# Kernel tuning notes

Hardware: AMD Instinct MI355X
Metric: run time of the kernel (lower is better)

Reference implementation:

```python
import jax, jax.numpy as jnp
import numpy as np
from jax import lax

D_MAX = 6.4; GRID_RES = 0.1; G = 9.81; MASS = 40.0
K_STIFF = 5000.0; K_DAMP = float(np.sqrt(4.0 * MASS * K_STIFF)); K_FRIC = 0.5
DT = 0.01; N_STEPS = 500; EPS = 1e-6


def _robot_geometry():
    # DPhysConfig.rigid_body_geometry(from_mesh=False), robot_size=(1.0, 0.5)
    xs = np.concatenate([np.linspace(-0.5, 0.5, 8), np.linspace(-0.5, 0.5, 8)])
    ys = np.concatenate([0.25 * np.ones(8), -0.25 * np.ones(8)])
    zz = np.array([0.2, 0.1, 0.0, 0.0, 0.0, 0.0, 0.1, 0.2])
    zs = np.concatenate([zz, zz])
    pts = np.stack([xs, ys, zs], 1).astype(np.float32)
    cog = pts.mean(0)
    return pts, (pts[:, 1] > cog[1]), (pts[:, 1] < cog[1])


def _inertia_inv(mass, pts):
    n = pts.shape[0]; mp = mass / n
    x, y, z = pts[:, 0], pts[:, 1], pts[:, 2]
    Ixx = (mp * (y**2 + z**2)).sum(); Iyy = (mp * (x**2 + z**2)).sum(); Izz = (mp * (x**2 + y**2)).sum()
    Ixy = -(mp * x * y).sum(); Ixz = -(mp * x * z).sum(); Iyz = -(mp * y * z).sum()
    I = np.array([[Ixx, Ixy, Ixz], [Ixy, Iyy, Iyz], [Ixz, Iyz, Izz]], dtype=np.float64) * 10.0
    return np.linalg.inv(I).astype(np.float32)


def _interp(grid, xq, yq):
    # bilinear interpolation of (B,H,W) grid at metric query points (B,N)
    B, H, W = grid.shape
    xi = jnp.clip((xq + D_MAX) / GRID_RES, 0.0, H - 2)
    yi = jnp.clip((yq + D_MAX) / GRID_RES, 0.0, W - 2)
    x0 = jnp.floor(xi).astype(jnp.int32); y0 = jnp.floor(yi).astype(jnp.int32)
    b = jnp.arange(B)[:, None]
    z00 = grid[b, x0, y0];     z10 = grid[b, x0 + 1, y0]
    z01 = grid[b, x0, y0 + 1]; z11 = grid[b, x0 + 1, y0 + 1]
    wx = xi - x0; wy = yi - y0
    return z00 * (1 - wx) * (1 - wy) + z10 * wx * (1 - wy) + z01 * (1 - wx) * wy + z11 * wx * wy


def _normals(grid, xq, yq):
    e = GRID_RES
    dzdx = (_interp(grid, xq + e, yq) - _interp(grid, xq - e, yq)) / (2 * e)
    dzdy = (_interp(grid, xq, yq + e) - _interp(grid, xq, yq - e)) / (2 * e)
    n = jnp.stack([-dzdx, -dzdy, jnp.ones_like(dzdx)], -1)
    return n / (jnp.linalg.norm(n, axis=-1, keepdims=True) + EPS)


def _skew(v):
    z = jnp.zeros_like(v[..., 0])
    return jnp.stack([
        jnp.stack([z, -v[..., 2], v[..., 1]], -1),
        jnp.stack([v[..., 2], z, -v[..., 0]], -1),
        jnp.stack([-v[..., 1], v[..., 0], z], -1)], -2)


def _rk4(x, xd, dt):
    k1 = dt * xd
    k2 = dt * (xd + k1 / 2)
    k3 = dt * (xd + k2 / 2)
    k4 = dt * (xd + k3)
    return x + (k1 + 2 * k2 + 2 * k3 + k4) / 6


def _integrate_rotation(R, omega, dt):
    Ox = _skew(omega)                                  # (B,3,3)
    theta = jnp.linalg.norm(omega, axis=-1)[:, None, None]
    Oxn = Ox / (theta + EPS)
    I3 = jnp.eye(3, dtype=R.dtype)
    return R @ (I3 + Oxn * jnp.sin(theta * dt) + (Oxn @ Oxn) * (1 - jnp.cos(theta * dt)))


def _forward_sim(z_grid, controls, robot_points, I_inv, mask_left, mask_right):
    B = z_grid.shape[0]; n_pts = robot_points.shape[0]
    dt = jnp.float32(DT)
    x = jnp.zeros((B, 3), z_grid.dtype).at[:, 2].set(1.0)
    xd = jnp.zeros((B, 3), z_grid.dtype)
    R = jnp.broadcast_to(jnp.eye(3, dtype=z_grid.dtype), (B, 3, 3))
    omega = jnp.zeros((B, 3), z_grid.dtype)
    x_points = x[:, None, :] + robot_points[None]      # (B,n,3)
    xd_points = jnp.zeros((B, n_pts, 3), z_grid.dtype)
    ml = mask_left[None, :, None]; mr = mask_right[None, :, None]

    def step(carry, u):
        x, xd, R, omega, x_points, xd_points = carry
        u_left, u_right = u[:, 0], u[:, 1]
        # --- forward_kinematics ---
        z_pts = _interp(z_grid, x_points[..., 0], x_points[..., 1])[..., None]
        dh = x_points[..., 2:3] - z_pts
        on_grid = ((x_points[..., 0:1] >= -D_MAX) & (x_points[..., 0:1] <= D_MAX) &
                   (x_points[..., 1:2] >= -D_MAX) & (x_points[..., 1:2] <= D_MAX))
        in_contact = ((dh <= 0.0) & on_grid).astype(x_points.dtype)
        n = _normals(z_grid, x_points[..., 0], x_points[..., 1])   # (B,n,3)
        xd_n = (xd_points * n).sum(-1, keepdims=True)
        F_spring = -(K_STIFF * dh + K_DAMP * xd_n) * n * in_contact
        thrust = R[..., 0]                                         # R @ [1,0,0]
        thrust = thrust / (jnp.linalg.norm(thrust, axis=-1, keepdims=True) + EPS)
        N = jnp.linalg.norm(F_spring, axis=2)[..., None]           # (B,n,1)
        v_l = (u_left[:, None] * thrust)[:, None, :]
        v_r = (u_right[:, None] * thrust)[:, None, :]
        f_l = K_FRIC * N * jnp.tanh(v_l - xd_points)
        f_r = K_FRIC * N * jnp.tanh(v_r - xd_points)
        F_fric = jnp.where(ml, f_l, jnp.where(mr, f_r, jnp.zeros_like(f_l)))
        r = x_points - x[:, None, :]
        torque = jnp.cross(r, F_spring + F_fric).sum(1)            # (B,3)
        omega_d = torque @ I_inv.T
        F_cog = jnp.array([0.0, 0.0, -MASS * G], z_grid.dtype) + F_spring.mean(1) + F_fric.mean(1)
        xdd = F_cog / MASS
        xd_pts_new = xd[:, None, :] + jnp.cross(omega[:, None, :], r)
        # --- update_state ---
        xd_new = _rk4(xd, xdd, dt)
        x_new = _rk4(x, xd_new, dt)
        x_points_new = _rk4(x_points, xd_pts_new, dt)
        omega_new = _rk4(omega, omega_d, dt)
        R_new = _integrate_rotation(R, omega_new, dt)
        carry_new = (x_new, xd_new, R_new, omega_new, x_points_new, xd_pts_new)
        out = jnp.concatenate([x_new, xd_new, omega_new, R_new.reshape(B, 9),
                               x_points_new.reshape(B, -1),
                               F_spring.reshape(B, -1), F_fric.reshape(B, -1)], -1)
        return carry_new, out

    _, traj = lax.scan(step, (x, xd, R, omega, x_points, xd_points),
                       jnp.swapaxes(controls, 0, 1))
    return jnp.swapaxes(traj, 0, 1)   # (B, T, 3+3+3+9+48+48+48=162)


def setup_inputs() -> dict:
    key = jax.random.key(0)
    k1, k2 = jax.random.split(key)
    B, H, W, T = 256, 128, 128, N_STEPS
    pts, ml, mr = _robot_geometry()
    z_grid = 0.1 * jax.random.normal(k1, (B, H, W), dtype=jnp.float32)
    controls = jax.random.uniform(k2, (B, T, 2), dtype=jnp.float32, minval=-1.2, maxval=1.2)
    return {
        "z_grid": z_grid,
        "controls": controls,
        "robot_points": jnp.asarray(pts),
        "I_inv": jnp.asarray(_inertia_inv(MASS, pts)),
        "mask_left": jnp.asarray(ml),
        "mask_right": jnp.asarray(mr),
    }


def reference(z_grid, controls, robot_points, I_inv, mask_left, mask_right):
    return _forward_sim(z_grid, controls, robot_points, I_inv, mask_left, mask_right)
```

## Files before the change

### kernel.cpp

```cpp
#include <hip/hip_runtime.h>
#include <math.h>

#define WGRID 128
#define HGRID 128
#define TSTEPS 500

__device__ __forceinline__ float dpp_sum16(float v) {
    int x;
    x = __builtin_amdgcn_update_dpp(0, __float_as_int(v), 0xB1, 0xF, 0xF, true);
    v += __int_as_float(x);
    x = __builtin_amdgcn_update_dpp(0, __float_as_int(v), 0x4E, 0xF, 0xF, true);
    v += __int_as_float(x);
    x = __builtin_amdgcn_update_dpp(0, __float_as_int(v), 0x141, 0xF, 0xF, true);
    v += __int_as_float(x);
    x = __builtin_amdgcn_update_dpp(0, __float_as_int(v), 0x140, 0xF, 0xF, true);
    v += __int_as_float(x);
    return v;
}

struct Ax { int i0; float w; };
__device__ __forceinline__ Ax axq(float q) {
    float xi = (q + 6.4f) / 0.1f;
    xi = fminf(fmaxf(xi, 0.0f), 126.0f);
    float f = floorf(xi);
    Ax a; a.i0 = (int)f; a.w = xi - f; return a;
}

struct Iq { float z00, z01, z10, z11, wx, wy; };
__device__ __forceinline__ Iq issueQ(const float* __restrict__ zb, Ax ax, Ax ay) {
    const float* r0 = zb + (ax.i0 * WGRID + ay.i0);
    Iq q;
    q.z00 = r0[0];
    q.z01 = r0[1];
    q.z10 = r0[WGRID];
    q.z11 = r0[WGRID + 1];
    q.wx = ax.w; q.wy = ay.w;
    return q;
}
__device__ __forceinline__ float combineQ(Iq q) {
    float ox = 1.0f - q.wx, oy = 1.0f - q.wy;
    return q.z00 * ox * oy + q.z10 * q.wx * oy + q.z01 * ox * q.wy + q.z11 * q.wx * q.wy;
}

extern "C" __global__ __launch_bounds__(64, 1) void dphys_sim(
    const float* __restrict__ z_grid,
    const float* __restrict__ controls,
    const float* __restrict__ robot_points,
    const float* __restrict__ I_inv,
    float* __restrict__ out)
{
    const int b = blockIdx.x;
    const int lane = threadIdx.x;

    const float* __restrict__ zb = z_grid + (size_t)b * (HGRID * WGRID);

    const float i00 = I_inv[0], i01 = I_inv[1], i02 = I_inv[2];
    const float i10 = I_inv[3], i11 = I_inv[4], i12 = I_inv[5];
    const float i20 = I_inv[6], i21 = I_inv[7], i22 = I_inv[8];

    const int p = lane & 15;
    const float rpx = robot_points[3 * p + 0];
    const float rpy = robot_points[3 * p + 1];
    const float rpz = robot_points[3 * p + 2];

    const float cog_y = dpp_sum16(rpy) * (1.0f / 16.0f);
    const bool is_left = rpy > cog_y;

    const float K_STIFF = 5000.0f;
    const float K_DAMP  = 894.4271909999159f;
    const float K_FRIC  = 0.5f;
    const float EPSF    = 1e-6f;
    const float CRK     = 0.010050166708416667f;

    float X = 0.f, Y = 0.f, Z = 1.f;
    float VX = 0.f, VY = 0.f, VZ = 0.f;
    float R00 = 1.f, R01 = 0.f, R02 = 0.f;
    float R10 = 0.f, R11 = 1.f, R12 = 0.f;
    float R20 = 0.f, R21 = 0.f, R22 = 1.f;
    float OX = 0.f, OY = 0.f, OZ = 0.f;
    float px = rpx, py = rpy, pz = rpz + 1.0f;
    float pvx = 0.f, pvy = 0.f, pvz = 0.f;

    float* outb = out + (size_t)b * TSTEPS * 162;
    const float* cg = controls + (size_t)b * (TSTEPS * 2);

    float u_l = cg[0], u_r = cg[1];

    Ax ax0 = axq(px), axp = axq(px + 0.1f), axm = axq(px - 0.1f);
    Ax ay0 = axq(py), ayp = axq(py + 0.1f), aym = axq(py - 0.1f);
    Iq qc  = issueQ(zb, ax0, ay0);
    Iq qxp = issueQ(zb, axp, ay0);
    Iq qxm = issueQ(zb, axm, ay0);
    Iq qyp = issueQ(zb, ax0, ayp);
    Iq qym = issueQ(zb, ax0, aym);

    #pragma unroll 1
    for (int t = 0; t < TSTEPS; ++t) {
        const int tn = (t + 1 < TSTEPS) ? (t + 1) : t;
        const float u_l_nxt = cg[2 * tn + 0];
        const float u_r_nxt = cg[2 * tn + 1];

        const float rx = px - X, ry = py - Y, rz = pz - Z;
        const float pvnx = VX + (OY * rz - OZ * ry);
        const float pvny = VY + (OZ * rx - OX * rz);
        const float pvnz = VZ + (OX * ry - OY * rx);
        const float pxn = fmaf(pvnx, CRK, px);
        const float pyn = fmaf(pvny, CRK, py);
        const float pzn = fmaf(pvnz, CRK, pz);

        Ax nax0 = axq(pxn), naxp = axq(pxn + 0.1f), naxm = axq(pxn - 0.1f);
        Ax nay0 = axq(pyn), nayp = axq(pyn + 0.1f), naym = axq(pyn - 0.1f);
        Iq nqc  = issueQ(zb, nax0, nay0);
        Iq nqxp = issueQ(zb, naxp, nay0);
        Iq nqxm = issueQ(zb, naxm, nay0);
        Iq nqyp = issueQ(zb, nax0, nayp);
        Iq nqym = issueQ(zb, nax0, naym);

        const float z_pt = combineQ(qc);
        const float zpx  = combineQ(qxp);
        const float zmx  = combineQ(qxm);
        const float zpy  = combineQ(qyp);
        const float zmy  = combineQ(qym);

        const float dh = pz - z_pt;
        const bool on = (px >= -6.4f) && (px <= 6.4f) && (py >= -6.4f) && (py <= 6.4f);
        const float contact = ((dh <= 0.0f) && on) ? 1.0f : 0.0f;

        const float dzdx = (zpx - zmx) / 0.2f;
        const float dzdy = (zpy - zmy) / 0.2f;
        float nx = -dzdx, ny = -dzdy, nz = 1.0f;
        const float nn = sqrtf(nx * nx + ny * ny + nz * nz) + EPSF;
        nx /= nn; ny /= nn; nz /= nn;

        const float xd_n = pvx * nx + pvy * ny + pvz * nz;
        const float s_mag = -(K_STIFF * dh + K_DAMP * xd_n);
        const float fsx = s_mag * nx * contact;
        const float fsy = s_mag * ny * contact;
        const float fsz = s_mag * nz * contact;

        const float Nmag = sqrtf(fsx * fsx + fsy * fsy + fsz * fsz);

        float tx = R00, ty = R10, tz = R20;
        const float tnn = sqrtf(tx * tx + ty * ty + tz * tz) + EPSF;
        tx /= tnn; ty /= tnn; tz /= tnn;

        const float u_sel = is_left ? u_l : u_r;
        const float kn = K_FRIC * Nmag;
        const float ffx = kn * tanhf(u_sel * tx - pvx);
        const float ffy = kn * tanhf(u_sel * ty - pvy);
        const float ffz = kn * tanhf(u_sel * tz - pvz);

        const float Fx = fsx + ffx, Fy = fsy + ffy, Fz = fsz + ffz;
        const float tqx = ry * Fz - rz * Fy;
        const float tqy = rz * Fx - rx * Fz;
        const float tqz = rx * Fy - ry * Fx;

        const float Tqx = dpp_sum16(tqx);
        const float Tqy = dpp_sum16(tqy);
        const float Tqz = dpp_sum16(tqz);
        const float Ssx = dpp_sum16(fsx);
        const float Ssy = dpp_sum16(fsy);
        const float Ssz = dpp_sum16(fsz);
        const float Sfx = dpp_sum16(ffx);
        const float Sfy = dpp_sum16(ffy);
        const float Sfz = dpp_sum16(ffz);

        const float odx = i00 * Tqx + i01 * Tqy + i02 * Tqz;
        const float ody = i10 * Tqx + i11 * Tqy + i12 * Tqz;
        const float odz = i20 * Tqx + i21 * Tqy + i22 * Tqz;

        const float Fcx = Ssx * 0.0625f + Sfx * 0.0625f;
        const float Fcy = Ssy * 0.0625f + Sfy * 0.0625f;
        const float Fcz = -392.4f + Ssz * 0.0625f + Sfz * 0.0625f;
        const float axd = Fcx / 40.0f;
        const float ayd = Fcy / 40.0f;
        const float azd = Fcz / 40.0f;

        const float VXn = fmaf(axd, CRK, VX);
        const float VYn = fmaf(ayd, CRK, VY);
        const float VZn = fmaf(azd, CRK, VZ);
        const float Xn = fmaf(VXn, CRK, X);
        const float Yn = fmaf(VYn, CRK, Y);
        const float Zn = fmaf(VZn, CRK, Z);
        const float OXn = fmaf(odx, CRK, OX);
        const float OYn = fmaf(ody, CRK, OY);
        const float OZn = fmaf(odz, CRK, OZ);

        const float th = sqrtf(OXn * OXn + OYn * OYn + OZn * OZn);
        const float tpe = th + EPSF;
        const float axn = OXn / tpe, ayn = OYn / tpe, azn = OZn / tpe;
        const float ang = th * 0.01f;
        const float sth = sinf(ang);
        const float cth = 1.0f - cosf(ang);
        const float M00 = 1.0f - (ayn * ayn + azn * azn) * cth;
        const float M01 = -azn * sth + axn * ayn * cth;
        const float M02 =  ayn * sth + axn * azn * cth;
        const float M10 =  azn * sth + axn * ayn * cth;
        const float M11 = 1.0f - (axn * axn + azn * azn) * cth;
        const float M12 = -axn * sth + ayn * azn * cth;
        const float M20 = -ayn * sth + axn * azn * cth;
        const float M21 =  axn * sth + ayn * azn * cth;
        const float M22 = 1.0f - (axn * axn + ayn * ayn) * cth;

        const float nR00 = R00 * M00 + R01 * M10 + R02 * M20;
        const float nR01 = R00 * M01 + R01 * M11 + R02 * M21;
        const float nR02 = R00 * M02 + R01 * M12 + R02 * M22;
        const float nR10 = R10 * M00 + R11 * M10 + R12 * M20;
        const float nR11 = R10 * M01 + R11 * M11 + R12 * M21;
        const float nR12 = R10 * M02 + R11 * M12 + R12 * M22;
        const float nR20 = R20 * M00 + R21 * M10 + R22 * M20;
        const float nR21 = R20 * M01 + R21 * M11 + R22 * M21;
        const float nR22 = R20 * M02 + R21 * M12 + R22 * M22;

        float* ob = outb + (size_t)t * 162;
        if (lane == 0) {
            ob[0] = Xn;  ob[1] = Yn;  ob[2] = Zn;
            ob[3] = VXn; ob[4] = VYn; ob[5] = VZn;
            ob[6] = OXn; ob[7] = OYn; ob[8] = OZn;
            ob[9]  = nR00; ob[10] = nR01; ob[11] = nR02;
            ob[12] = nR10; ob[13] = nR11; ob[14] = nR12;
            ob[15] = nR20; ob[16] = nR21; ob[17] = nR22;
        }
        if (lane < 16) {
            float* o1 = ob + 18 + 3 * lane;
            o1[0] = pxn; o1[1] = pyn; o1[2] = pzn;
            float* o2 = ob + 66 + 3 * lane;
            o2[0] = fsx; o2[1] = fsy; o2[2] = fsz;
            float* o3 = ob + 114 + 3 * lane;
            o3[0] = ffx; o3[1] = ffy; o3[2] = ffz;
        }

        X = Xn; Y = Yn; Z = Zn;
        VX = VXn; VY = VYn; VZ = VZn;
        px = pxn; py = pyn; pz = pzn;
        pvx = pvnx; pvy = pvny; pvz = pvnz;
        OX = OXn; OY = OYn; OZ = OZn;
        R00 = nR00; R01 = nR01; R02 = nR02;
        R10 = nR10; R11 = nR11; R12 = nR12;
        R20 = nR20; R21 = nR21; R22 = nR22;
        qc = nqc; qxp = nqxp; qxm = nqxm; qyp = nqyp; qym = nqym;
        u_l = u_l_nxt; u_r = u_r_nxt;
    }
}

extern "C" void kernel_launch(void* const* d_in, const int* in_sizes, int n_in,
                              void* d_out, int out_size, void* d_ws, size_t ws_size,
                              hipStream_t stream) {
    const float* z_grid       = (const float*)d_in[0];
    const float* controls     = (const float*)d_in[1];
    const float* robot_points = (const float*)d_in[2];
    const float* I_inv        = (const float*)d_in[3];
    float* out = (float*)d_out;

    const int B = in_sizes[0] / (HGRID * WGRID);
    dphys_sim<<<dim3(B), dim3(64), 0, stream>>>(z_grid, controls, robot_points, I_inv, out);
}
```

Before: 920.5 us.

## Stage per-batch height grid in LDS and vectorize state stores

Copies the whole 128x128 height grid for each batch element into 64 KB of shared memory at kernel start, so the per-step bilinear gathers read LDS instead of global/L2. This targets the latency of the serial 500-step loop, where each step waits on dependent gathers. It also unrolls the time loop by two and writes the 18 rigid-body state values as float2 pairs. The cost is an upfront 64 KB load per block and higher LDS use per block, which may limit how many blocks share a CU.

```diff
diff --git a/kernel.cpp b/kernel.cpp
--- a/kernel.cpp
+++ b/kernel.cpp
@@ -27,8 +27,8 @@
 }
 
 struct Iq { float z00, z01, z10, z11, wx, wy; };
-__device__ __forceinline__ Iq issueQ(const float* __restrict__ zb, Ax ax, Ax ay) {
-    const float* r0 = zb + (ax.i0 * WGRID + ay.i0);
+__device__ __forceinline__ Iq issueQ(const float* __restrict__ sg, Ax ax, Ax ay) {
+    const float* r0 = sg + (ax.i0 * WGRID + ay.i0);
     Iq q;
     q.z00 = r0[0];
     q.z01 = r0[1];
@@ -49,10 +49,17 @@
     const float* __restrict__ I_inv,
     float* __restrict__ out)
 {
+    __shared__ float sg[HGRID * WGRID];
+
     const int b = blockIdx.x;
     const int lane = threadIdx.x;
 
-    const float* __restrict__ zb = z_grid + (size_t)b * (HGRID * WGRID);
+    {
+        const float4* src = (const float4*)(z_grid + (size_t)b * (HGRID * WGRID));
+        float4* dst = (float4*)sg;
+        #pragma unroll 4
+        for (int i = lane; i < (HGRID * WGRID) / 4; i += 64) dst[i] = src[i];
+    }
 
     const float i00 = I_inv[0], i01 = I_inv[1], i02 = I_inv[2];
     const float i10 = I_inv[3], i11 = I_inv[4], i12 = I_inv[5];
@@ -65,6 +72,8 @@
 
     const float cog_y = dpp_sum16(rpy) * (1.0f / 16.0f);
     const bool is_left = rpy > cog_y;
+
+    __syncthreads();
 
     const float K_STIFF = 5000.0f;
     const float K_DAMP  = 894.4271909999159f;
@@ -88,13 +97,13 @@
 
     Ax ax0 = axq(px), axp = axq(px + 0.1f), axm = axq(px - 0.1f);
     Ax ay0 = axq(py), ayp = axq(py + 0.1f), aym = axq(py - 0.1f);
-    Iq qc  = issueQ(zb, ax0, ay0);
-    Iq qxp = issueQ(zb, axp, ay0);
-    Iq qxm = issueQ(zb, axm, ay0);
-    Iq qyp = issueQ(zb, ax0, ayp);
-    Iq qym = issueQ(zb, ax0, aym);
-
-    #pragma unroll 1
+    Iq qc  = issueQ(sg, ax0, ay0);
+    Iq qxp = issueQ(sg, axp, ay0);
+    Iq qxm = issueQ(sg, axm, ay0);
+    Iq qyp = issueQ(sg, ax0, ayp);
+    Iq qym = issueQ(sg, ax0, aym);
+
+    #pragma unroll 2
     for (int t = 0; t < TSTEPS; ++t) {
         const int tn = (t + 1 < TSTEPS) ? (t + 1) : t;
         const float u_l_nxt = cg[2 * tn + 0];
@@ -110,11 +119,11 @@
 
         Ax nax0 = axq(pxn), naxp = axq(pxn + 0.1f), naxm = axq(pxn - 0.1f);
         Ax nay0 = axq(pyn), nayp = axq(pyn + 0.1f), naym = axq(pyn - 0.1f);
-        Iq nqc  = issueQ(zb, nax0, nay0);
-        Iq nqxp = issueQ(zb, naxp, nay0);
-        Iq nqxm = issueQ(zb, naxm, nay0);
-        Iq nqyp = issueQ(zb, nax0, nayp);
-        Iq nqym = issueQ(zb, nax0, naym);
+        Iq nqc  = issueQ(sg, nax0, nay0);
+        Iq nqxp = issueQ(sg, naxp, nay0);
+        Iq nqxm = issueQ(sg, naxm, nay0);
+        Iq nqyp = issueQ(sg, nax0, nayp);
+        Iq nqym = issueQ(sg, nax0, naym);
 
         const float z_pt = combineQ(qc);
         const float zpx  = combineQ(qxp);
@@ -214,12 +223,16 @@
 
         float* ob = outb + (size_t)t * 162;
         if (lane == 0) {
-            ob[0] = Xn;  ob[1] = Yn;  ob[2] = Zn;
-            ob[3] = VXn; ob[4] = VYn; ob[5] = VZn;
-            ob[6] = OXn; ob[7] = OYn; ob[8] = OZn;
-            ob[9]  = nR00; ob[10] = nR01; ob[11] = nR02;
-            ob[12] = nR10; ob[13] = nR11; ob[14] = nR12;
-            ob[15] = nR20; ob[16] = nR21; ob[17] = nR22;
+            float2* ob2 = (float2*)ob;
+            ob2[0] = make_float2(Xn,  Yn);
+            ob2[1] = make_float2(Zn,  VXn);
+            ob2[2] = make_float2(VYn, VZn);
+            ob2[3] = make_float2(OXn, OYn);
+            ob2[4] = make_float2(OZn, nR00);
+            ob2[5] = make_float2(nR01, nR02);
+            ob2[6] = make_float2(nR10, nR11);
+            ob2[7] = make_float2(nR12, nR20);
+            ob2[8] = make_float2(nR21, nR22);
         }
         if (lane < 16) {
             float* o1 = ob + 18 + 3 * lane;
```

Result: faster. 872.1 us (-5.3%).
